# Performance work log

Hardware: AMD Instinct MI355X
Metric: run time of the kernel (lower is better)

## Reference

```python
import jax, jax.numpy as jnp
import numpy as np

B, L, E, H, D = 2, 2048, 2048, 16, 128
EPS = 1e-6


def _rms(x, scale):
    # RMSNorm over head_dim, computed in float32 (matches torch RMSNorm)
    x32 = x.astype(jnp.float32)
    n = jnp.mean(x32 * x32, axis=-1, keepdims=True)
    return (scale.astype(jnp.float32) * (x32 * jax.lax.rsqrt(n + EPS))).astype(x.dtype)


def _rotary(x, rope):
    # x: [B, L, H, D]; rope: [B, L, D//2, 2]
    xs = x.astype(jnp.float32).reshape(*x.shape[:-1], -1, 2)  # [B,L,H,D/2,2]
    rc = rope.reshape(xs.shape[0], xs.shape[1], 1, xs.shape[3], 2).astype(jnp.float32)
    out = jnp.stack(
        [xs[..., 0] * rc[..., 0] - xs[..., 1] * rc[..., 1],
         xs[..., 1] * rc[..., 0] + xs[..., 0] * rc[..., 1]], -1)
    return out.reshape(x.shape).astype(x.dtype)


def setup_inputs() -> dict:
    key = jax.random.key(0)
    ks = jax.random.split(key, 9)
    s = 0.02  # weight init scale (~kaiming fan_in for E=2048)
    return {
        "inputs_q": jax.random.normal(ks[0], (B, L, E), jnp.float32),
        "inputs_kv": jax.random.normal(ks[1], (B, L, E), jnp.float32),
        "bias": jax.random.normal(ks[2], (B, 1, L, L), jnp.float32),
        "rope_q": jax.random.normal(ks[3], (B, L, D // 2, 2), jnp.float32),
        "rope_k": jax.random.normal(ks[4], (B, L, D // 2, 2), jnp.float32),
        "Wq": jax.random.normal(ks[5], (E, E), jnp.float32) * s,
        "Wk": jax.random.normal(ks[6], (E, E), jnp.float32) * s,
        "Wv": jax.random.normal(ks[7], (E, E), jnp.float32) * s,
        "Wo": jax.random.normal(ks[8], (E, E), jnp.float32) * s,
        "q_scale": jnp.ones((D,), jnp.float32),
        "k_scale": jnp.ones((D,), jnp.float32),
    }


def reference(inputs_q, inputs_kv, bias, rope_q, rope_k, Wq, Wk, Wv, Wo, q_scale, k_scale):
    Bq, Lq, _ = inputs_q.shape
    Lk = inputs_kv.shape[1]
    dtype = inputs_q.dtype
    # QKV projections (torch Linear: y = x @ W.T)
    q = (inputs_q @ Wq.T).reshape(Bq, Lq, H, D)
    k = (inputs_kv @ Wk.T).reshape(Bq, Lk, H, D)
    v = (inputs_kv @ Wv.T).reshape(Bq, Lk, H, D)
    # qk_norm
    q = _rms(q, q_scale)
    k = _rms(k, k_scale)
    # rotary embeddings
    q = _rotary(q, rope_q)
    k = _rotary(k, rope_k)
    # float32_logits
    q = q.astype(jnp.float32)
    k = k.astype(jnp.float32)
    # faithful to torch source: query.div_(depth ** (-0.5)) == q * sqrt(D)
    q = q / (D ** (-0.5))
    logits = jnp.einsum('bqhd,bkhd->bhqk', q, k) + bias.astype(jnp.float32)
    probs = jax.nn.softmax(logits, axis=-1).astype(dtype)
    # dropout_rate = 0.0 -> identity
    x = jnp.einsum('bhqk,bkhd->bqhd', probs, v).reshape(Bq, Lq, E)
    return x @ Wo.T
```

## Files before the change

kernel.cpp:

```cpp
#include <hip/hip_runtime.h>

#define Bb 2
#define Ll 2048
#define Ee 2048
#define Hh 16
#define Dd 128
#define BL (Bb * Ll)
#define LOSCALE 1024.0f
#define INV_LOSCALE (1.0f / 1024.0f)

typedef float f32x4 __attribute__((ext_vector_type(4)));
typedef _Float16 f16x8 __attribute__((ext_vector_type(8)));

__device__ __forceinline__ void gld_lds16(const void* g, void* l) {
  __builtin_amdgcn_global_load_lds((const __attribute__((address_space(1))) void*)g,
                                   (__attribute__((address_space(3))) void*)l, 16, 0, 0);
}

__global__ __launch_bounds__(256) void cvt_f32_f16(const float* __restrict__ in,
                                                   _Float16* __restrict__ out, int n4) {
  int i = blockIdx.x * 256 + threadIdx.x;
  if (i < n4) {
    float4 f = ((const float4*)in)[i];
    _Float16 o[4] = {(_Float16)f.x, (_Float16)f.y, (_Float16)f.z, (_Float16)f.w};
    ((uint2*)out)[i] = *(uint2*)o;
  }
}

__global__ __launch_bounds__(256) void cvt_split(const float* __restrict__ in,
                                                 _Float16* __restrict__ hi,
                                                 _Float16* __restrict__ lo, int n4) {
  int i = blockIdx.x * 256 + threadIdx.x;
  if (i < n4) {
    float4 f = ((const float4*)in)[i];
    float fa[4] = {f.x, f.y, f.z, f.w};
    _Float16 h[4], l[4];
    for (int j = 0; j < 4; ++j) {
      h[j] = (_Float16)fa[j];
      l[j] = (_Float16)((fa[j] - (float)h[j]) * LOSCALE);
    }
    ((uint2*)hi)[i] = *(uint2*)h;
    ((uint2*)lo)[i] = *(uint2*)l;
  }
}

template <typename OutT>
__global__ __launch_bounds__(256, 2) void gemm_bt(const _Float16* __restrict__ A,
                                                  const _Float16* __restrict__ Bw,
                                                  OutT* __restrict__ C, int M, int N, int K) {
  __shared__ _Float16 As[128 * 64];
  __shared__ _Float16 Bs[128 * 64];
  const int tid = threadIdx.x;
  const int wave = tid >> 6, lane = tid & 63;
  const int quad = lane >> 4, l16 = lane & 15;
  const int lrow = lane >> 3, lch = lane & 7;
  const int scol = (lch ^ lrow) * 8;
  const int bm = blockIdx.y * 128, bn = blockIdx.x * 128;
  const int wm = (wave >> 1) * 64, wn = (wave & 1) * 64;

  f32x4 acc[4][4] = {};

  for (int k0 = 0; k0 < K; k0 += 64) {
    for (int i = 0; i < 4; ++i) {
      int br = wave * 32 + i * 8;
      gld_lds16(&A[(size_t)(bm + br + lrow) * K + k0 + scol], &As[br * 64]);
      gld_lds16(&Bw[(size_t)(bn + br + lrow) * K + k0 + scol], &Bs[br * 64]);
    }
    __syncthreads();
    for (int ks = 0; ks < 2; ++ks) {
      f16x8 af[4], bf[4];
      for (int mt = 0; mt < 4; ++mt)
        af[mt] = *(const f16x8*)&As[(wm + mt * 16 + l16) * 64 +
                                    (((ks * 4 + quad) ^ (l16 & 7)) * 8)];
      for (int nt = 0; nt < 4; ++nt)
        bf[nt] = *(const f16x8*)&Bs[(wn + nt * 16 + l16) * 64 +
                                    (((ks * 4 + quad) ^ (l16 & 7)) * 8)];
      for (int mt = 0; mt < 4; ++mt)
        for (int nt = 0; nt < 4; ++nt)
          acc[mt][nt] = __builtin_amdgcn_mfma_f32_16x16x32_f16(af[mt], bf[nt], acc[mt][nt], 0, 0, 0);
    }
    __syncthreads();
  }

  for (int mt = 0; mt < 4; ++mt)
    for (int nt = 0; nt < 4; ++nt)
      for (int r = 0; r < 4; ++r) {
        int m = bm + wm + mt * 16 + quad * 4 + r;
        int n = bn + wn + nt * 16 + l16;
        C[(size_t)m * N + n] = (OutT)acc[mt][nt][r];
      }
}

__global__ __launch_bounds__(256, 2) void gemm_bt_split(
    const _Float16* __restrict__ Ah, const _Float16* __restrict__ Al,
    const _Float16* __restrict__ Bh, const _Float16* __restrict__ Bl,
    float* __restrict__ C, int M, int N, int K) {
  __shared__ _Float16 Ash[128 * 64];
  __shared__ _Float16 Asl[128 * 64];
  __shared__ _Float16 Bsh[128 * 64];
  __shared__ _Float16 Bsl[128 * 64];
  const int tid = threadIdx.x;
  const int wave = tid >> 6, lane = tid & 63;
  const int quad = lane >> 4, l16 = lane & 15;
  const int lrow = lane >> 3, lch = lane & 7;
  const int scol = (lch ^ lrow) * 8;
  const int bm = blockIdx.y * 128, bn = blockIdx.x * 128;
  const int wm = (wave >> 1) * 64, wn = (wave & 1) * 64;

  f32x4 acc_hh[4][4] = {};
  f32x4 acc_cr[4][4] = {};

  for (int k0 = 0; k0 < K; k0 += 64) {
    for (int i = 0; i < 4; ++i) {
      int br = wave * 32 + i * 8;
      size_t ga = (size_t)(bm + br + lrow) * K + k0 + scol;
      size_t gb = (size_t)(bn + br + lrow) * K + k0 + scol;
      gld_lds16(&Ah[ga], &Ash[br * 64]);
      gld_lds16(&Al[ga], &Asl[br * 64]);
      gld_lds16(&Bh[gb], &Bsh[br * 64]);
      gld_lds16(&Bl[gb], &Bsl[br * 64]);
    }
    __syncthreads();
    for (int ks = 0; ks < 2; ++ks) {
      const int sw = ((ks * 4 + quad) ^ (l16 & 7)) * 8;
      f16x8 afh[4], afl[4], bfh[4], bfl[4];
      for (int mt = 0; mt < 4; ++mt) {
        afh[mt] = *(const f16x8*)&Ash[(wm + mt * 16 + l16) * 64 + sw];
        afl[mt] = *(const f16x8*)&Asl[(wm + mt * 16 + l16) * 64 + sw];
      }
      for (int nt = 0; nt < 4; ++nt) {
        bfh[nt] = *(const f16x8*)&Bsh[(wn + nt * 16 + l16) * 64 + sw];
        bfl[nt] = *(const f16x8*)&Bsl[(wn + nt * 16 + l16) * 64 + sw];
      }
      for (int mt = 0; mt < 4; ++mt)
        for (int nt = 0; nt < 4; ++nt) {
          acc_hh[mt][nt] = __builtin_amdgcn_mfma_f32_16x16x32_f16(afh[mt], bfh[nt], acc_hh[mt][nt], 0, 0, 0);
          acc_cr[mt][nt] = __builtin_amdgcn_mfma_f32_16x16x32_f16(afh[mt], bfl[nt], acc_cr[mt][nt], 0, 0, 0);
          acc_cr[mt][nt] = __builtin_amdgcn_mfma_f32_16x16x32_f16(afl[mt], bfh[nt], acc_cr[mt][nt], 0, 0, 0);
        }
    }
    __syncthreads();
  }

  for (int mt = 0; mt < 4; ++mt)
    for (int nt = 0; nt < 4; ++nt)
      for (int r = 0; r < 4; ++r) {
        int m = bm + wm + mt * 16 + quad * 4 + r;
        int n = bn + wn + nt * 16 + l16;
        C[(size_t)m * N + n] = acc_hh[mt][nt][r] + acc_cr[mt][nt][r] * INV_LOSCALE;
      }
}

__global__ __launch_bounds__(256) void transpose_v(const _Float16* __restrict__ V,
                                                   _Float16* __restrict__ Vt) {
  __shared__ _Float16 T[64][72];
  const int bl0 = blockIdx.x * 64, n0 = blockIdx.y * 64;
  const int tid = threadIdx.x;
  for (int c = 0; c < 2; ++c) {
    int chunk = tid + c * 256;
    int r = chunk >> 3, cc = (chunk & 7) * 8;
    *(uint4*)&T[r][cc] = *(const uint4*)&V[(size_t)(bl0 + r) * Ee + n0 + cc];
  }
  __syncthreads();
  const int b = bl0 >> 11;
  const int k0 = bl0 & (Ll - 1);
  for (int c = 0; c < 2; ++c) {
    int chunk = tid + c * 256;
    int nr = chunk >> 3, kc = (chunk & 7) * 8;
    _Float16 tmp[8];
    for (int j = 0; j < 8; ++j) tmp[j] = T[kc + j][nr];
    *(uint4*)&Vt[((size_t)b * Ee + n0 + nr) * Ll + k0 + kc] = *(uint4*)tmp;
  }
}

__global__ __launch_bounds__(256) void rmsrope(const float* __restrict__ raw,
                                               const float* __restrict__ scale,
                                               const float* __restrict__ rope,
                                               _Float16* __restrict__ outh,
                                               _Float16* __restrict__ outl, float outmul) {
  int row = blockIdx.x * 4 + (threadIdx.x >> 6);
  int t = threadIdx.x & 63;
  float2 x = *(const float2*)&raw[(size_t)row * Dd + 2 * t];
  float ss = x.x * x.x + x.y * x.y;
  for (int off = 1; off < 64; off <<= 1) ss += __shfl_xor(ss, off);
  float inv = rsqrtf(ss * (1.0f / Dd) + 1e-6f);
  float2 sc = *(const float2*)&scale[2 * t];
  float y0 = x.x * inv * sc.x;
  float y1 = x.y * inv * sc.y;
  int bl = row >> 4;
  float2 cs = *(const float2*)&rope[(size_t)bl * Dd + 2 * t];
  float r0 = (y0 * cs.x - y1 * cs.y) * outmul;
  float r1 = (y1 * cs.x + y0 * cs.y) * outmul;
  _Float16 h[2] = {(_Float16)r0, (_Float16)r1};
  _Float16 l[2] = {(_Float16)((r0 - (float)h[0]) * LOSCALE),
                   (_Float16)((r1 - (float)h[1]) * LOSCALE)};
  *(uint*)&outh[(size_t)row * Dd + 2 * t] = *(uint*)h;
  *(uint*)&outl[(size_t)row * Dd + 2 * t] = *(uint*)l;
}

__global__ __launch_bounds__(256, 2) void attn(const _Float16* __restrict__ Qh_,
                                               const _Float16* __restrict__ Ql_,
                                               const _Float16* __restrict__ Kh_,
                                               const _Float16* __restrict__ Kl_,
                                               const _Float16* __restrict__ Vt_g,
                                               const _Float16* __restrict__ bias16,
                                               _Float16* __restrict__ O) {
  __shared__ _Float16 Ksh[64 * 128];
  __shared__ _Float16 Ksl[64 * 128];
  __shared__ _Float16 Vts[128 * 64];
  __shared__ _Float16 Ps[128][72];

  const int tid = threadIdx.x;
  const int wave = tid >> 6, lane = tid & 63;
  const int quad = lane >> 4, l16 = lane & 15;
  const int lrow8 = lane >> 3, lch8 = lane & 7;
  const int lrow16 = lane >> 4, lch16 = lane & 15;
  const int h = blockIdx.x;
  const int q0 = blockIdx.y * 128;
  const int b = blockIdx.z;

  f16x8 aqh[2][4], aql[2][4];
  for (int t = 0; t < 2; ++t) {
    size_t qrow = (((size_t)b * Ll + q0 + wave * 32 + t * 16 + l16) * Hh + h) * Dd;
    for (int ks = 0; ks < 4; ++ks) {
      aqh[t][ks] = *(const f16x8*)&Qh_[qrow + ks * 32 + quad * 8];
      aql[t][ks] = *(const f16x8*)&Ql_[qrow + ks * 32 + quad * 8];
    }
  }
  const _Float16* Vbase = Vt_g + ((size_t)b * Ee + h * Dd) * Ll;
  const _Float16* biasb = bias16 + (size_t)b * Ll * Ll;

  f32x4 o_acc[2][8] = {};
  float m_r[2][4], l_r[2][4];
  for (int t = 0; t < 2; ++t)
    for (int r = 0; r < 4; ++r) { m_r[t][r] = -1e30f; l_r[t][r] = 0.f; }

  for (int kt = 0; kt < Ll / 64; ++kt) {
    const int k0 = kt * 64;
    for (int i = 0; i < 4; ++i) {
      int br = wave * 16 + i * 4;
      int row = br + lrow16;
      int sc = (lch16 ^ (row & 7)) * 8;
      size_t g = (((size_t)b * Ll + k0 + row) * Hh + h) * Dd + sc;
      gld_lds16(&Kh_[g], &Ksh[br * 128]);
      gld_lds16(&Kl_[g], &Ksl[br * 128]);
    }
    for (int i = 0; i < 4; ++i) {
      int br = wave * 32 + i * 8;
      int row = br + lrow8;
      int sc = (lch8 ^ (row & 7)) * 8;
      gld_lds16(&Vbase[(size_t)row * Ll + k0 + sc], &Vts[br * 64]);
    }
    __syncthreads();

    f32x4 s_hh[2][4] = {}, s_cr[2][4] = {};
    for (int ks = 0; ks < 4; ++ks) {
      const int sw = ((ks * 4 + quad) ^ (l16 & 7)) * 8;
      for (int nt = 0; nt < 4; ++nt) {
        f16x8 bkh = *(const f16x8*)&Ksh[(nt * 16 + l16) * 128 + sw];
        f16x8 bkl = *(const f16x8*)&Ksl[(nt * 16 + l16) * 128 + sw];
        for (int t = 0; t < 2; ++t) {
          s_hh[t][nt] = __builtin_amdgcn_mfma_f32_16x16x32_f16(aqh[t][ks], bkh, s_hh[t][nt], 0, 0, 0);
          s_cr[t][nt] = __builtin_amdgcn_mfma_f32_16x16x32_f16(aqh[t][ks], bkl, s_cr[t][nt], 0, 0, 0);
          s_cr[t][nt] = __builtin_amdgcn_mfma_f32_16x16x32_f16(aql[t][ks], bkh, s_cr[t][nt], 0, 0, 0);
        }
      }
    }

    for (int t = 0; t < 2; ++t) {
      f32x4 sv[4];
      for (int nt = 0; nt < 4; ++nt)
        for (int r = 0; r < 4; ++r) {
          int gq = q0 + wave * 32 + t * 16 + quad * 4 + r;
          int gk = k0 + nt * 16 + l16;
          sv[nt][r] = s_hh[t][nt][r] + s_cr[t][nt][r] * INV_LOSCALE +
                      (float)biasb[(size_t)gq * Ll + gk];
        }
      float alpha[4];
      for (int r = 0; r < 4; ++r) {
        float x = fmaxf(fmaxf(sv[0][r], sv[1][r]), fmaxf(sv[2][r], sv[3][r]));
        for (int off = 1; off < 16; off <<= 1) x = fmaxf(x, __shfl_xor(x, off));
        float mn = fmaxf(m_r[t][r], x);
        alpha[r] = __expf(m_r[t][r] - mn);
        m_r[t][r] = mn;
      }
      for (int r = 0; r < 4; ++r) {
        float sum = 0.f;
        for (int nt = 0; nt < 4; ++nt) {
          float p = __expf(sv[nt][r] - m_r[t][r]);
          sum += p;
          Ps[wave * 32 + t * 16 + quad * 4 + r][nt * 16 + l16] = (_Float16)p;
        }
        for (int off = 1; off < 16; off <<= 1) sum += __shfl_xor(sum, off);
        l_r[t][r] = l_r[t][r] * alpha[r] + sum;
      }
      for (int ot = 0; ot < 8; ++ot)
        for (int r = 0; r < 4; ++r) o_acc[t][ot][r] *= alpha[r];
    }

    for (int ks = 0; ks < 2; ++ks) {
      const int sw = ((ks * 4 + quad) ^ (l16 & 7)) * 8;
      f16x8 ap[2];
      for (int t = 0; t < 2; ++t)
        ap[t] = *(const f16x8*)&Ps[wave * 32 + t * 16 + l16][ks * 32 + quad * 8];
      for (int ot = 0; ot < 8; ++ot) {
        f16x8 bv = *(const f16x8*)&Vts[(ot * 16 + l16) * 64 + sw];
        for (int t = 0; t < 2; ++t)
          o_acc[t][ot] = __builtin_amdgcn_mfma_f32_16x16x32_f16(ap[t], bv, o_acc[t][ot], 0, 0, 0);
      }
    }
    __syncthreads();
  }

  for (int t = 0; t < 2; ++t)
    for (int ot = 0; ot < 8; ++ot)
      for (int r = 0; r < 4; ++r) {
        int m = q0 + wave * 32 + t * 16 + quad * 4 + r;
        O[(((size_t)b * Ll + m) * Hh + h) * Dd + ot * 16 + l16] =
            (_Float16)(o_acc[t][ot][r] / l_r[t][r]);
      }
}

extern "C" void kernel_launch(void* const* d_in, const int* in_sizes, int n_in,
                              void* d_out, int out_size, void* d_ws, size_t ws_size,
                              hipStream_t stream) {
  const float* inputs_q  = (const float*)d_in[0];
  const float* inputs_kv = (const float*)d_in[1];
  const float* bias      = (const float*)d_in[2];
  const float* rope_q    = (const float*)d_in[3];
  const float* rope_k    = (const float*)d_in[4];
  const float* Wq        = (const float*)d_in[5];
  const float* Wk        = (const float*)d_in[6];
  const float* Wv        = (const float*)d_in[7];
  const float* Wo        = (const float*)d_in[8];
  const float* q_scale   = (const float*)d_in[9];
  const float* k_scale   = (const float*)d_in[10];
  float* out = (float*)d_out;

  char* ws = (char*)d_ws;
  size_t o = 0;
  auto alloc = [&](size_t bytes) {
    char* p = ws + o;
    o += (bytes + 255) & ~(size_t)255;
    return p;
  };
  const size_t szX16 = (size_t)BL * Ee * 2;
  const size_t szW16 = (size_t)Ee * Ee * 2;
  _Float16* Xq_hi  = (_Float16*)alloc(szX16);
  _Float16* Xq_lo  = (_Float16*)alloc(szX16);
  _Float16* Xkv_hi = (_Float16*)alloc(szX16);
  _Float16* Xkv_lo = (_Float16*)alloc(szX16);
  _Float16* Wq_hi  = (_Float16*)alloc(szW16);
  _Float16* Wq_lo  = (_Float16*)alloc(szW16);
  _Float16* Wk_hi  = (_Float16*)alloc(szW16);
  _Float16* Wk_lo  = (_Float16*)alloc(szW16);
  _Float16* Wv_hi  = (_Float16*)alloc(szW16);
  _Float16* Wo_hi  = (_Float16*)alloc(szW16);
  float* Qraw = (float*)alloc((size_t)BL * Ee * 4);
  float* Kraw = (float*)alloc((size_t)BL * Ee * 4);
  _Float16* V16 = (_Float16*)alloc(szX16);
  _Float16* Q16h   = Xq_hi;
  _Float16* Q16l   = Xq_lo;
  _Float16* K16h   = Xkv_hi;
  _Float16* K16l   = Xkv_lo;
  _Float16* X16    = (_Float16*)Qraw;
  _Float16* Vt_g   = Wq_hi;
  _Float16* bias16 = (_Float16*)Kraw;

  const int nX4 = BL * Ee / 4;
  const int nW4 = Ee * Ee / 4;
  const int nB4 = Bb * Ll * Ll / 4;
  cvt_split<<<nX4 / 256, 256, 0, stream>>>(inputs_q, Xq_hi, Xq_lo, nX4);
  cvt_split<<<nX4 / 256, 256, 0, stream>>>(inputs_kv, Xkv_hi, Xkv_lo, nX4);
  cvt_split<<<nW4 / 256, 256, 0, stream>>>(Wq, Wq_hi, Wq_lo, nW4);
  cvt_split<<<nW4 / 256, 256, 0, stream>>>(Wk, Wk_hi, Wk_lo, nW4);
  cvt_f32_f16<<<nW4 / 256, 256, 0, stream>>>(Wv, Wv_hi, nW4);
  cvt_f32_f16<<<nW4 / 256, 256, 0, stream>>>(Wo, Wo_hi, nW4);

  dim3 gblk(Ee / 128, BL / 128);
  gemm_bt_split<<<gblk, 256, 0, stream>>>(Xq_hi, Xq_lo, Wq_hi, Wq_lo, Qraw, BL, Ee, Ee);
  gemm_bt_split<<<gblk, 256, 0, stream>>>(Xkv_hi, Xkv_lo, Wk_hi, Wk_lo, Kraw, BL, Ee, Ee);
  gemm_bt<_Float16><<<gblk, 256, 0, stream>>>(Xkv_hi, Wv_hi, V16, BL, Ee, Ee);

  transpose_v<<<dim3(BL / 64, Ee / 64), 256, 0, stream>>>(V16, Vt_g);

  rmsrope<<<BL * Hh / 4, 256, 0, stream>>>(Qraw, q_scale, rope_q, Q16h, Q16l, sqrtf((float)Dd));
  rmsrope<<<BL * Hh / 4, 256, 0, stream>>>(Kraw, k_scale, rope_k, K16h, K16l, 1.0f);

  cvt_f32_f16<<<nB4 / 256, 256, 0, stream>>>(bias, bias16, nB4);

  attn<<<dim3(Hh, Ll / 128, Bb), 256, 0, stream>>>(Q16h, Q16l, K16h, K16l, Vt_g, bias16, X16);

  gemm_bt<float><<<gblk, 256, 0, stream>>>(X16, Wo_hi, out, BL, Ee, Ee);
}
```

Baseline: 814.1 us.

## Use 8 waves per attention block and stage bias tiles via LDS async loads

The attention kernel moves from 4 waves with two 16-row q tiles each to 8 waves with one 16-row tile each (512 threads). This halves per-thread accumulator and register state and raises the occupancy hint. Bias tiles are now loaded into the P scratch buffer in shared memory with global_load_lds instead of scattered per-element global reads. The trade-off is that K/V loads are now spread over more waves, and the P buffer reuse needs care about the bias/P layout overlap within each wave's slice.

```diff
diff --git a/kernel.cpp b/kernel.cpp
--- a/kernel.cpp
+++ b/kernel.cpp
@@ -198,7 +198,7 @@
   *(uint*)&outl[(size_t)row * Dd + 2 * t] = *(uint*)l;
 }
 
-__global__ __launch_bounds__(256, 2) void attn(const _Float16* __restrict__ Qh_,
+__global__ __launch_bounds__(512, 4) void attn(const _Float16* __restrict__ Qh_,
                                                const _Float16* __restrict__ Ql_,
                                                const _Float16* __restrict__ Kh_,
                                                const _Float16* __restrict__ Kl_,
@@ -208,7 +208,7 @@
   __shared__ _Float16 Ksh[64 * 128];
   __shared__ _Float16 Ksl[64 * 128];
   __shared__ _Float16 Vts[128 * 64];
-  __shared__ _Float16 Ps[128][72];
+  __shared__ _Float16 Ps[128 * 72];
 
   const int tid = threadIdx.x;
   const int wave = tid >> 6, lane = tid & 63;
@@ -219,106 +219,97 @@
   const int q0 = blockIdx.y * 128;
   const int b = blockIdx.z;
 
-  f16x8 aqh[2][4], aql[2][4];
-  for (int t = 0; t < 2; ++t) {
-    size_t qrow = (((size_t)b * Ll + q0 + wave * 32 + t * 16 + l16) * Hh + h) * Dd;
+  f16x8 aqh[4], aql[4];
+  {
+    size_t qrow = (((size_t)b * Ll + q0 + wave * 16 + l16) * Hh + h) * Dd;
     for (int ks = 0; ks < 4; ++ks) {
-      aqh[t][ks] = *(const f16x8*)&Qh_[qrow + ks * 32 + quad * 8];
-      aql[t][ks] = *(const f16x8*)&Ql_[qrow + ks * 32 + quad * 8];
+      aqh[ks] = *(const f16x8*)&Qh_[qrow + ks * 32 + quad * 8];
+      aql[ks] = *(const f16x8*)&Ql_[qrow + ks * 32 + quad * 8];
     }
   }
   const _Float16* Vbase = Vt_g + ((size_t)b * Ee + h * Dd) * Ll;
   const _Float16* biasb = bias16 + (size_t)b * Ll * Ll;
 
-  f32x4 o_acc[2][8] = {};
-  float m_r[2][4], l_r[2][4];
-  for (int t = 0; t < 2; ++t)
-    for (int r = 0; r < 4; ++r) { m_r[t][r] = -1e30f; l_r[t][r] = 0.f; }
+  f32x4 o_acc[8] = {};
+  float m_r[4], l_r[4];
+  for (int r = 0; r < 4; ++r) { m_r[r] = -1e30f; l_r[r] = 0.f; }
 
   for (int kt = 0; kt < Ll / 64; ++kt) {
     const int k0 = kt * 64;
-    for (int i = 0; i < 4; ++i) {
-      int br = wave * 16 + i * 4;
+    for (int i = 0; i < 2; ++i) {
+      int br = wave * 8 + i * 4;
       int row = br + lrow16;
       int sc = (lch16 ^ (row & 7)) * 8;
       size_t g = (((size_t)b * Ll + k0 + row) * Hh + h) * Dd + sc;
       gld_lds16(&Kh_[g], &Ksh[br * 128]);
       gld_lds16(&Kl_[g], &Ksl[br * 128]);
     }
-    for (int i = 0; i < 4; ++i) {
-      int br = wave * 32 + i * 8;
+    for (int i = 0; i < 2; ++i) {
+      int br = wave * 16 + i * 8;
       int row = br + lrow8;
       int sc = (lch8 ^ (row & 7)) * 8;
       gld_lds16(&Vbase[(size_t)row * Ll + k0 + sc], &Vts[br * 64]);
     }
-    __syncthreads();
-
-    f32x4 s_hh[2][4] = {}, s_cr[2][4] = {};
+    for (int i = 0; i < 2; ++i) {
+      int gq = q0 + wave * 16 + i * 8 + lrow8;
+      gld_lds16(&biasb[(size_t)gq * Ll + k0 + lch8 * 8], &Ps[wave * 1152 + i * 512]);
+    }
+    __syncthreads();
+
+    f32x4 s_hh[4] = {}, s_cr[4] = {};
     for (int ks = 0; ks < 4; ++ks) {
       const int sw = ((ks * 4 + quad) ^ (l16 & 7)) * 8;
       for (int nt = 0; nt < 4; ++nt) {
         f16x8 bkh = *(const f16x8*)&Ksh[(nt * 16 + l16) * 128 + sw];
         f16x8 bkl = *(const f16x8*)&Ksl[(nt * 16 + l16) * 128 + sw];
-        for (int t = 0; t < 2; ++t) {
-          s_hh[t][nt] = __builtin_amdgcn_mfma_f32_16x16x32_f16(aqh[t][ks], bkh, s_hh[t][nt], 0, 0, 0);
-          s_cr[t][nt] = __builtin_amdgcn_mfma_f32_16x16x32_f16(aqh[t][ks], bkl, s_cr[t][nt], 0, 0, 0);
-          s_cr[t][nt] = __builtin_amdgcn_mfma_f32_16x16x32_f16(aql[t][ks], bkh, s_cr[t][nt], 0, 0, 0);
-        }
-      }
-    }
-
-    for (int t = 0; t < 2; ++t) {
-      f32x4 sv[4];
-      for (int nt = 0; nt < 4; ++nt)
-        for (int r = 0; r < 4; ++r) {
-          int gq = q0 + wave * 32 + t * 16 + quad * 4 + r;
-          int gk = k0 + nt * 16 + l16;
-          sv[nt][r] = s_hh[t][nt][r] + s_cr[t][nt][r] * INV_LOSCALE +
-                      (float)biasb[(size_t)gq * Ll + gk];
-        }
-      float alpha[4];
-      for (int r = 0; r < 4; ++r) {
-        float x = fmaxf(fmaxf(sv[0][r], sv[1][r]), fmaxf(sv[2][r], sv[3][r]));
-        for (int off = 1; off < 16; off <<= 1) x = fmaxf(x, __shfl_xor(x, off));
-        float mn = fmaxf(m_r[t][r], x);
-        alpha[r] = __expf(m_r[t][r] - mn);
-        m_r[t][r] = mn;
-      }
-      for (int r = 0; r < 4; ++r) {
-        float sum = 0.f;
-        for (int nt = 0; nt < 4; ++nt) {
-          float p = __expf(sv[nt][r] - m_r[t][r]);
-          sum += p;
-          Ps[wave * 32 + t * 16 + quad * 4 + r][nt * 16 + l16] = (_Float16)p;
-        }
-        for (int off = 1; off < 16; off <<= 1) sum += __shfl_xor(sum, off);
-        l_r[t][r] = l_r[t][r] * alpha[r] + sum;
-      }
-      for (int ot = 0; ot < 8; ++ot)
-        for (int r = 0; r < 4; ++r) o_acc[t][ot][r] *= alpha[r];
-    }
+        s_hh[nt] = __builtin_amdgcn_mfma_f32_16x16x32_f16(aqh[ks], bkh, s_hh[nt], 0, 0, 0);
+        s_cr[nt] = __builtin_amdgcn_mfma_f32_16x16x32_f16(aqh[ks], bkl, s_cr[nt], 0, 0, 0);
+        s_cr[nt] = __builtin_amdgcn_mfma_f32_16x16x32_f16(aql[ks], bkh, s_cr[nt], 0, 0, 0);
+      }
+    }
+    for (int nt = 0; nt < 4; ++nt)
+      for (int r = 0; r < 4; ++r)
+        s_hh[nt][r] += s_cr[nt][r] * INV_LOSCALE +
+                       (float)Ps[wave * 1152 + (quad * 4 + r) * 64 + nt * 16 + l16];
+
+    float alpha[4];
+    for (int r = 0; r < 4; ++r) {
+      float x = fmaxf(fmaxf(s_hh[0][r], s_hh[1][r]), fmaxf(s_hh[2][r], s_hh[3][r]));
+      for (int off = 1; off < 16; off <<= 1) x = fmaxf(x, __shfl_xor(x, off));
+      float mn = fmaxf(m_r[r], x);
+      alpha[r] = __expf(m_r[r] - mn);
+      m_r[r] = mn;
+    }
+    for (int r = 0; r < 4; ++r) {
+      float sum = 0.f;
+      for (int nt = 0; nt < 4; ++nt) {
+        float p = __expf(s_hh[nt][r] - m_r[r]);
+        sum += p;
+        Ps[(wave * 16 + quad * 4 + r) * 72 + nt * 16 + l16] = (_Float16)p;
+      }
+      for (int off = 1; off < 16; off <<= 1) sum += __shfl_xor(sum, off);
+      l_r[r] = l_r[r] * alpha[r] + sum;
+    }
+    for (int ot = 0; ot < 8; ++ot)
+      for (int r = 0; r < 4; ++r) o_acc[ot][r] *= alpha[r];
 
     for (int ks = 0; ks < 2; ++ks) {
       const int sw = ((ks * 4 + quad) ^ (l16 & 7)) * 8;
-      f16x8 ap[2];
-      for (int t = 0; t < 2; ++t)
-        ap[t] = *(const f16x8*)&Ps[wave * 32 + t * 16 + l16][ks * 32 + quad * 8];
+      f16x8 ap = *(const f16x8*)&Ps[(wave * 16 + l16) * 72 + ks * 32 + quad * 8];
       for (int ot = 0; ot < 8; ++ot) {
         f16x8 bv = *(const f16x8*)&Vts[(ot * 16 + l16) * 64 + sw];
-        for (int t = 0; t < 2; ++t)
-          o_acc[t][ot] = __builtin_amdgcn_mfma_f32_16x16x32_f16(ap[t], bv, o_acc[t][ot], 0, 0, 0);
-      }
-    }
-    __syncthreads();
-  }
-
-  for (int t = 0; t < 2; ++t)
-    for (int ot = 0; ot < 8; ++ot)
-      for (int r = 0; r < 4; ++r) {
-        int m = q0 + wave * 32 + t * 16 + quad * 4 + r;
-        O[(((size_t)b * Ll + m) * Hh + h) * Dd + ot * 16 + l16] =
-            (_Float16)(o_acc[t][ot][r] / l_r[t][r]);
-      }
+        o_acc[ot] = __builtin_amdgcn_mfma_f32_16x16x32_f16(ap, bv, o_acc[ot], 0, 0, 0);
+      }
+    }
+    __syncthreads();
+  }
+
+  for (int ot = 0; ot < 8; ++ot)
+    for (int r = 0; r < 4; ++r) {
+      int m = q0 + wave * 16 + quad * 4 + r;
+      O[(((size_t)b * Ll + m) * Hh + h) * Dd + ot * 16 + l16] =
+          (_Float16)(o_acc[ot][r] / l_r[r]);
+    }
 }
 
 extern "C" void kernel_launch(void* const* d_in, const int* in_sizes, int n_in,
@@ -389,7 +380,7 @@
 
   cvt_f32_f16<<<nB4 / 256, 256, 0, stream>>>(bias, bias16, nB4);
 
-  attn<<<dim3(Hh, Ll / 128, Bb), 256, 0, stream>>>(Q16h, Q16l, K16h, K16l, Vt_g, bias16, X16);
+  attn<<<dim3(Hh, Ll / 128, Bb), 512, 0, stream>>>(Q16h, Q16l, K16h, K16l, Vt_g, bias16, X16);
 
   gemm_bt<float><<<gblk, 256, 0, stream>>>(X16, Wo_hi, out, BL, Ee, Ee);
 }
```

New measurement: 779.8 us. 4.2% less time.
